# Kernel optimization log

Hardware: AMD Instinct MI355X
Metric: run time of the kernel (lower is better)

## Reference

```python
import jax, jax.numpy as jnp
import numpy as np
import math

B, L, D = 4, 4096, 512
P, V = 128, 8  # n_phases, value_dim
PI = math.pi

def _lin(x, w, b):
    return x @ w + b

def _gelu(x):
    return jax.nn.gelu(x, approximate=False)  # torch default exact GELU

def setup_inputs() -> dict:
    key = jax.random.key(0)
    ks = iter(jax.random.split(key, 32))
    def rn(shape, scale=0.02):
        return (jax.random.normal(next(ks), shape, dtype=jnp.float32) * scale)
    inp = {
        'x': jax.random.normal(next(ks), (B, L, D), dtype=jnp.float32),
        'pos_phases': jax.random.normal(next(ks), (L, D), dtype=jnp.float32) * PI,
        'magnitude_scale': jnp.float32(5.0),
        'w_v': rn((D, D)), 'b_v': jnp.zeros((D,), jnp.float32),
        'w_o': rn((D, D)), 'b_o': jnp.zeros((D,), jnp.float32),
        'w_m': rn((D, D)), 'b_m': jnp.zeros((D,), jnp.float32),
        'w_q': rn((D, D)), 'b_q': jnp.zeros((D,), jnp.float32),
        'w_ke': rn((D, P)), 'b_ke': jnp.zeros((P,), jnp.float32),
        'w_ve': rn((D, V)), 'b_ve': jnp.zeros((V,), jnp.float32),
        'w_s1': rn((2 * D, D)), 'b_s1': jnp.zeros((D,), jnp.float32),
        'w_s2': rn((D, P)), 'b_s2': jnp.zeros((P,), jnp.float32),
        'w_g': rn((D, 1)), 'b_g': jnp.zeros((1,), jnp.float32),
        'w_kv': rn((V, D)), 'b_kv': jnp.zeros((D,), jnp.float32),
        'ln_g': jnp.ones((2 * D,), jnp.float32), 'ln_b': jnp.zeros((2 * D,), jnp.float32),
        'w_t1': rn((2 * D, 2 * D)), 'b_t1': jnp.zeros((2 * D,), jnp.float32),
        'w_t2': rn((2 * D, D)), 'b_t2': jnp.zeros((D,), jnp.float32),
    }
    return inp

def _forward(x, pos_phases, magnitude_scale, w_v, b_v, w_o, b_o, w_m, b_m,
             w_q, b_q, w_ke, b_ke, w_ve, b_ve, w_s1, b_s1, w_s2, b_s2,
             w_g, b_g, w_kv, b_kv, ln_g, ln_b, w_t1, b_t1, w_t2, b_t2):
    b, l, d = x.shape
    phi = pos_phases[:l]                               # [L,D]
    cos_phi, sin_phi = jnp.cos(phi), jnp.sin(phi)
    # --- positional phasor memory ---
    v1 = _lin(x, w_v, b_v)                             # [B,L,D]
    magnitude = jax.nn.sigmoid(_lin(x, w_m, b_m)) * jnp.abs(magnitude_scale)
    weighted_v1 = magnitude * v1
    mem1_cos = jnp.cumsum(weighted_v1 * cos_phi, axis=1)
    mem1_sin = jnp.cumsum(weighted_v1 * sin_phi, axis=1)
    sqrt_mag = jnp.sqrt(jnp.cumsum(magnitude, axis=1) + 1e-8)
    mem1_cos = mem1_cos / sqrt_mag
    mem1_sin = mem1_sin / sqrt_mag
    phi_query = phi + _lin(x, w_q, b_q)
    pos_ret = (mem1_cos * jnp.cos(phi_query) + mem1_sin * jnp.sin(phi_query)) / math.sqrt(d)
    pos_out = _lin(pos_ret, w_o, b_o)                  # [B,L,D]
    # --- key-value phasor memory ---
    query_phase = jnp.tanh(_lin(x, w_ke, b_ke)) * PI   # [B,L,P]
    values = _lin(x, w_ve, b_ve)                       # [B,L,V]
    store_gate = jax.nn.sigmoid(_lin(x, w_g, b_g))     # [B,L,1]
    positions = jnp.arange(1, l + 1, dtype=x.dtype)[None, :, None]
    context_avg = jnp.cumsum(x, axis=1) / positions
    sk = _lin(_gelu(_lin(jnp.concatenate([x, context_avg], axis=-1), w_s1, b_s1)), w_s2, b_s2)
    storage_phase = jnp.tanh(sk) * PI                  # [B,L,P]
    gv = values * store_gate                           # [B,L,V]
    kv_bound_cos = jnp.cos(storage_phase)[..., None] * gv[:, :, None, :]  # [B,L,P,V]
    kv_bound_sin = jnp.sin(storage_phase)[..., None] * gv[:, :, None, :]
    kv_mem_cos = jnp.cumsum(kv_bound_cos, axis=1)
    kv_mem_sin = jnp.cumsum(kv_bound_sin, axis=1)
    gate_cumsum = jnp.clip(jnp.cumsum(store_gate, axis=1), 1.0, None)     # [B,L,1]
    inv = 1.0 / jnp.sqrt(gate_cumsum)[..., None]
    kv_mem_cos = kv_mem_cos * inv
    kv_mem_sin = kv_mem_sin * inv
    kv_retrieved = (jnp.cos(query_phase)[..., None] * kv_mem_cos
                    + jnp.sin(query_phase)[..., None] * kv_mem_sin).sum(axis=2) / math.sqrt(P)
    kv_out = _lin(kv_retrieved, w_kv, b_kv)            # [B,L,D]
    # --- output projection (dropout = eval/identity) ---
    combined = jnp.concatenate([pos_out, kv_out], axis=-1)  # [B,L,2D]
    mu = combined.mean(axis=-1, keepdims=True)
    var = combined.var(axis=-1, keepdims=True)
    ln = (combined - mu) / jnp.sqrt(var + 1e-5) * ln_g + ln_b
    return x + _lin(_gelu(_lin(ln, w_t1, b_t1)), w_t2, b_t2)

def reference(x, pos_phases, magnitude_scale, w_v, b_v, w_o, b_o, w_m, b_m,
              w_q, b_q, w_ke, b_ke, w_ve, b_ve, w_s1, b_s1, w_s2, b_s2,
              w_g, b_g, w_kv, b_kv, ln_g, ln_b, w_t1, b_t1, w_t2, b_t2):
    return _forward(x, pos_phases, magnitude_scale, w_v, b_v, w_o, b_o, w_m, b_m,
                    w_q, b_q, w_ke, b_ke, w_ve, b_ve, w_s1, b_s1, w_s2, b_s2,
                    w_g, b_g, w_kv, b_kv, ln_g, ln_b, w_t1, b_t1, w_t2, b_t2)
```

## Files before the change

### kernel.cpp

```cpp
#include <hip/hip_runtime.h>
#include <math.h>

#define NTOK 16384
#define LSEQ 4096
#define BATCH 4
#define DDIM 512
#define PDIM 128
#define VDIM 8
#define PI_F 3.14159265358979323846f

#define NC2 64
#define CL2 64
#define NC3 128
#define CL3 32

#define VMQ_S 1536

typedef __attribute__((ext_vector_type(8))) short bfrag8;
typedef __attribute__((ext_vector_type(4))) float facc4;

__device__ __forceinline__ float sigmoid_(float v) { return 1.0f / (1.0f + expf(-v)); }
__device__ __forceinline__ float gelu_(float v) { return 0.5f * v * (1.0f + erff(v * 0.70710678118654752f)); }

__device__ __forceinline__ unsigned short f2bf(float f) {
    unsigned int u = __builtin_bit_cast(unsigned int, f);
    u += 0x7fffu + ((u >> 16) & 1u);
    return (unsigned short)(u >> 16);
}
__device__ __forceinline__ float bf2f(unsigned short h) {
    return __builtin_bit_cast(float, ((unsigned int)h) << 16);
}
__device__ __forceinline__ float bflo(unsigned int w) { return __builtin_bit_cast(float, w << 16); }
__device__ __forceinline__ float bfhi(unsigned int w) { return __builtin_bit_cast(float, w & 0xffff0000u); }

__device__ __forceinline__ void async16(const unsigned short* g, unsigned short* l) {
    __builtin_amdgcn_global_load_lds(
        (const __attribute__((address_space(1))) unsigned int*)g,
        (__attribute__((address_space(3))) unsigned int*)l, 16, 0, 0);
}

__global__ __launch_bounds__(256) void gemm_bf16(
    const unsigned short* __restrict__ A, int ldA,
    const unsigned short* __restrict__ Wt,
    const float* __restrict__ bias, int K,
    float* __restrict__ Cf, unsigned short* __restrict__ Cb, int ldC, int colOff,
    const float* __restrict__ res, int ldRes,
    int act)
{
    __shared__ __align__(16) unsigned short Asm[2][128 * 64];
    __shared__ __align__(16) unsigned short Bsm[2][128 * 64];
    const int tid = threadIdx.x;
    const int lane = tid & 63;
    const int wv = tid >> 6;
    const int wm = wv & 1, wn = wv >> 1;
    const int quad = lane >> 4, cc = lane & 15;

    const int C = gridDim.x, R = gridDim.y;
    const int bid = blockIdx.x + C * blockIdx.y;
    const int xcd = bid & 7;
    const int s = bid >> 3;
    const int by = xcd * (R >> 3) + s / C;
    const int bx = s - (s / C) * C;
    const int row0 = by << 7;
    const int col0 = bx << 7;

    facc4 acc[4][4];
#pragma unroll
    for (int i = 0; i < 4; ++i)
#pragma unroll
        for (int j = 0; j < 4; ++j) acc[i][j] = (facc4){0.f, 0.f, 0.f, 0.f};

    const int nk = K >> 6;

    int srow[4]; int soff[4]; int sdst[4];
#pragma unroll
    for (int k = 0; k < 4; ++k) {
        int g = tid + k * 256;
        int r = g >> 3, sd = g & 7;
        srow[k] = r;
        soff[k] = (sd ^ (r & 7)) * 8;
        sdst[k] = g * 8;
    }

    auto stage = [&](int t, int buf) {
        const int koff = t << 6;
#pragma unroll
        for (int k = 0; k < 4; ++k) {
            async16(A  + (size_t)(row0 + srow[k]) * ldA + koff + soff[k], &Asm[buf][sdst[k]]);
            async16(Wt + (size_t)(col0 + srow[k]) * K   + koff + soff[k], &Bsm[buf][sdst[k]]);
        }
    };

    stage(0, 0);

    const int swz = cc & 7;
    int cur = 0;
    for (int t = 0; t < nk; ++t) {
        if (t + 1 < nk) {
            stage(t + 1, cur ^ 1);
            asm volatile("s_waitcnt vmcnt(8)" ::: "memory");
        } else {
            asm volatile("s_waitcnt vmcnt(0)" ::: "memory");
        }
        __builtin_amdgcn_s_barrier();
        __builtin_amdgcn_sched_barrier(0);
#pragma unroll
        for (int kk = 0; kk < 2; ++kk) {
            const int sl = ((kk * 4 + quad) ^ swz) * 8;
            bfrag8 afr[4], bfr[4];
#pragma unroll
            for (int mt = 0; mt < 4; ++mt)
                afr[mt] = *(const bfrag8*)&Asm[cur][(wm * 64 + mt * 16 + cc) * 64 + sl];
#pragma unroll
            for (int nt = 0; nt < 4; ++nt)
                bfr[nt] = *(const bfrag8*)&Bsm[cur][(wn * 64 + nt * 16 + cc) * 64 + sl];
#pragma unroll
            for (int mt = 0; mt < 4; ++mt)
#pragma unroll
                for (int nt = 0; nt < 4; ++nt)
                    acc[mt][nt] = __builtin_amdgcn_mfma_f32_16x16x32_bf16(
                        afr[mt], bfr[nt], acc[mt][nt], 0, 0, 0);
        }
        asm volatile("s_waitcnt lgkmcnt(0)" ::: "memory");
        __builtin_amdgcn_s_barrier();
        cur ^= 1;
    }

#pragma unroll
    for (int nt = 0; nt < 4; ++nt) {
        int col = col0 + wn * 64 + nt * 16 + cc;
        float bvv = bias[col];
#pragma unroll
        for (int mt = 0; mt < 4; ++mt) {
            int rowb = row0 + wm * 64 + mt * 16 + quad * 4;
#pragma unroll
            for (int r = 0; r < 4; ++r) {
                float v = acc[mt][nt][r] + bvv;
                if (act == 1) v = gelu_(v);
                size_t row = (size_t)(rowb + r);
                if (res) v += res[row * ldRes + col];
                size_t idx = row * ldC + colOff + col;
                if (Cf) Cf[idx] = v;
                else    Cb[idx] = f2bf(v);
            }
        }
    }
}

__global__ __launch_bounds__(256) void k_wcvt_all(
    const float* __restrict__ w_v, const float* __restrict__ w_m,
    const float* __restrict__ w_q, const float* __restrict__ w_o,
    const float* __restrict__ w_ke, const float* __restrict__ w_s1,
    const float* __restrict__ w_s2, const float* __restrict__ w_t1,
    const float* __restrict__ w_t2, unsigned short* __restrict__ WT,
    const float* __restrict__ b_v, const float* __restrict__ b_m,
    const float* __restrict__ b_q, float* __restrict__ cbias)
{
    const int bid = blockIdx.x;
    const int tid = threadIdx.x;
    if (bid >= 3200) {
        int i = (bid - 3200) * 256 + tid;
        if (i < 512) cbias[i] = b_v[i];
        else if (i < 1024) cbias[i] = b_m[i - 512];
        else cbias[i] = b_q[i - 1024];
        return;
    }
    const float* W; int K, N; unsigned short* Wt; int l;
    if (bid < 1024) {
        K = 512; N = 512;
        int seg = bid >> 8; l = bid & 255;
        W = (seg == 0) ? w_v : (seg == 1) ? w_m : (seg == 2) ? w_q : w_o;
        Wt = WT + seg * 262144;
    } else if (bid < 1088) { W = w_ke; K = 512;  N = 128;  Wt = WT + 1048576; l = bid - 1024; }
    else if (bid < 1600)   { W = w_s1; K = 1024; N = 512;  Wt = WT + 1114112; l = bid - 1088; }
    else if (bid < 1664)   { W = w_s2; K = 512;  N = 128;  Wt = WT + 1638400; l = bid - 1600; }
    else if (bid < 2688)   { W = w_t1; K = 1024; N = 1024; Wt = WT + 1703936; l = bid - 1664; }
    else                   { W = w_t2; K = 1024; N = 512;  Wt = WT + 2752512; l = bid - 2688; }
    const int ntx = N >> 5;
    const int bx = l % ntx, by = l / ntx;
    __shared__ float t[32][33];
    const int tx = tid & 31, ty = tid >> 5;
#pragma unroll
    for (int r = 0; r < 4; ++r) {
        int k = by * 32 + ty + r * 8;
        t[ty + r * 8][tx] = W[(size_t)k * N + bx * 32 + tx];
    }
    __syncthreads();
#pragma unroll
    for (int r = 0; r < 4; ++r) {
        int n = bx * 32 + ty + r * 8;
        Wt[(size_t)n * K + by * 32 + tx] = f2bf(t[tx][ty + r * 8]);
    }
}

__global__ void k_xcvt(const float* __restrict__ x, unsigned short* __restrict__ xcat)
{
    int g = blockIdx.x * 256 + threadIdx.x;
    int c8 = (g & 63) * 8, r = g >> 6;
    const float4* xp = (const float4*)(x + (size_t)r * 512 + c8);
    float4 a = xp[0], b = xp[1];
    uint4 o;
    o.x = (unsigned int)f2bf(a.x) | ((unsigned int)f2bf(a.y) << 16);
    o.y = (unsigned int)f2bf(a.z) | ((unsigned int)f2bf(a.w) << 16);
    o.z = (unsigned int)f2bf(b.x) | ((unsigned int)f2bf(b.y) << 16);
    o.w = (unsigned int)f2bf(b.z) | ((unsigned int)f2bf(b.w) << 16);
    *(uint4*)&xcat[(size_t)r * 1024 + c8] = o;
}

__global__ void k_phi(const float* __restrict__ pp, float* __restrict__ cphi,
                      float* __restrict__ sphi, int n)
{
    int i = blockIdx.x * 256 + threadIdx.x;
    if (i < n) {
        float s, c;
        sincosf(pp[i], &s, &c);
        cphi[i] = c;
        sphi[i] = s;
    }
}

__global__ __launch_bounds__(256) void k_glin(const float* __restrict__ x,
                                              const float* __restrict__ wg,
                                              const float* __restrict__ bg,
                                              float* __restrict__ glin)
{
    int wid = threadIdx.x >> 6, lane = threadIdx.x & 63;
    int row = blockIdx.x * 4 + wid;
    const float4* xr = (const float4*)(x + (size_t)row * DDIM);
    const float4* w4 = (const float4*)wg;
    float4 a0 = xr[lane], a1 = xr[lane + 64];
    float4 w0 = w4[lane], w1 = w4[lane + 64];
    float p = a0.x * w0.x + a0.y * w0.y + a0.z * w0.z + a0.w * w0.w
            + a1.x * w1.x + a1.y * w1.y + a1.z * w1.z + a1.w * w1.w;
    for (int d = 32; d >= 1; d >>= 1) p += __shfl_down(p, d, 64);
    if (lane == 0) glin[row] = p + bg[0];
}

__global__ __launch_bounds__(256) void k_values(const float* __restrict__ x,
                                                const float* __restrict__ wve,
                                                const float* __restrict__ bve,
                                                const float* __restrict__ glin,
                                                float* __restrict__ gv)
{
    int g = blockIdx.x * 256 + threadIdx.x;
    int m = g & 7, r = g >> 3;
    const float4* xr = (const float4*)(x + (size_t)r * DDIM);
    float acc = bve[m];
    for (int kq = 0; kq < 128; ++kq) {
        float4 a = xr[kq];
        int k = kq * 4;
        acc += a.x * wve[k * 8 + m] + a.y * wve[(k + 1) * 8 + m]
             + a.z * wve[(k + 2) * 8 + m] + a.w * wve[(k + 3) * 8 + m];
    }
    gv[g] = acc * sigmoid_(glin[r]);
}

__global__ __launch_bounds__(256) void k_scan1a(
    const unsigned short* __restrict__ vmq, const float* __restrict__ x,
    const float* __restrict__ cphi, const float* __restrict__ sphi,
    const float* __restrict__ msp, float* __restrict__ sum2)
{
    int g = blockIdx.x * 256 + threadIdx.x;
    int d = g & 511;
    int rest = g >> 9;
    int chunk = rest & (NC2 - 1);
    int b = rest >> 6;
    float msabs = fabsf(msp[0]);
    size_t row = (size_t)b * LSEQ + chunk * CL2;
    const unsigned short* vp = vmq + row * VMQ_S + d;
    const float* xp = x + row * DDIM + d;
    size_t pbase = ((size_t)chunk * CL2) * DDIM + d;
    float ac = 0.f, as = 0.f, am = 0.f, ax = 0.f;
    for (int i = 0; i < CL2; ++i) {
        float vv = bf2f(vp[0]);
        float ml = bf2f(vp[512]);
        float xv = xp[0];
        float cp = cphi[pbase], sp = sphi[pbase];
        float mag = msabs * sigmoid_(ml);
        float wv = mag * vv;
        ac += wv * cp; as += wv * sp; am += mag; ax += xv;
        vp += VMQ_S; xp += DDIM; pbase += DDIM;
    }
    int col = (b * DDIM + d) * NC2 + chunk;
    sum2[0 * 131072 + col] = ac;
    sum2[1 * 131072 + col] = as;
    sum2[2 * 131072 + col] = am;
    sum2[3 * 131072 + col] = ax;
}

__global__ __launch_bounds__(256) void k_scan1b(float* __restrict__ sum2)
{
    int g = blockIdx.x * 256 + threadIdx.x;
    float* p = sum2 + (size_t)g * NC2;
    float run = 0.f;
    for (int i = 0; i < NC2; ++i) { float t = p[i]; p[i] = run; run += t; }
}

__global__ __launch_bounds__(256) void k_scan1c(
    const unsigned short* __restrict__ vmq, const float* __restrict__ x,
    const float* __restrict__ cphi, const float* __restrict__ sphi,
    const float* __restrict__ msp, const float* __restrict__ sum2,
    unsigned short* __restrict__ pret, unsigned short* __restrict__ xcat)
{
    int g = blockIdx.x * 256 + threadIdx.x;
    int d = g & 511;
    int rest = g >> 9;
    int chunk = rest & (NC2 - 1);
    int b = rest >> 6;
    float msabs = fabsf(msp[0]);
    int col = (b * DDIM + d) * NC2 + chunk;
    float ac = sum2[col];
    float as = sum2[131072 + col];
    float am = sum2[2 * 131072 + col];
    float ax = sum2[3 * 131072 + col];
    size_t row = (size_t)b * LSEQ + chunk * CL2;
    const unsigned short* vp = vmq + row * VMQ_S + d;
    size_t base = row * DDIM + d;
    size_t pbase = ((size_t)chunk * CL2) * DDIM + d;
    int l = chunk * CL2;
    const float rsd = 0.04419417382415922f;
    for (int i = 0; i < CL2; ++i, ++l) {
        float vv = bf2f(vp[0]);
        float ml = bf2f(vp[512]);
        float q = bf2f(vp[1024]);
        float xv = x[base];
        float cp = cphi[pbase], sp = sphi[pbase];
        float mag = msabs * sigmoid_(ml);
        float wv = mag * vv;
        ac += wv * cp; as += wv * sp; am += mag; ax += xv;
        float inv = rsqrtf(am + 1e-8f);
        float mc = ac * inv, msn = as * inv;
        float cq, sq;
        sincosf(q, &sq, &cq);
        float cpq = cp * cq - sp * sq;
        float spq = sp * cq + cp * sq;
        pret[base] = f2bf((mc * cpq + msn * spq) * rsd);
        size_t orow = (size_t)b * LSEQ + l;
        xcat[orow * 1024 + 512 + d] = f2bf(ax / (float)(l + 1));
        vp += VMQ_S; base += DDIM; pbase += DDIM;
    }
}

__global__ void k_phases(const float* __restrict__ sk, const unsigned short* __restrict__ ke,
                         unsigned short* __restrict__ csp, unsigned short* __restrict__ ssp,
                         unsigned short* __restrict__ cqp, unsigned short* __restrict__ sqp, int n)
{
    int g = blockIdx.x * 256 + threadIdx.x;
    if (g < n) {
        float s, c;
        float spv = tanhf(sk[g]) * PI_F;
        sincosf(spv, &s, &c);
        csp[g] = f2bf(c); ssp[g] = f2bf(s);
        float qpv = tanhf(bf2f(ke[g])) * PI_F;
        sincosf(qpv, &s, &c);
        cqp[g] = f2bf(c); sqp[g] = f2bf(s);
    }
}

__global__ __launch_bounds__(1024) void k_gatescan(const float* __restrict__ glin,
                                                   float* __restrict__ gcum)
{
    __shared__ float s[1024];
    int b = blockIdx.x, tid = threadIdx.x;
    const float* gp = glin + (size_t)b * LSEQ + tid * 4;
    float e0 = sigmoid_(gp[0]);
    float e1 = sigmoid_(gp[1]);
    float e2 = sigmoid_(gp[2]);
    float e3 = sigmoid_(gp[3]);
    float l0 = e0, l1 = l0 + e1, l2 = l1 + e2, l3 = l2 + e3;
    s[tid] = l3;
    __syncthreads();
    for (int off = 1; off < 1024; off <<= 1) {
        float t = (tid >= off) ? s[tid - off] : 0.0f;
        __syncthreads();
        s[tid] += t;
        __syncthreads();
    }
    float excl = s[tid] - l3;
    float* out = gcum + (size_t)b * LSEQ + tid * 4;
    out[0] = excl + l0; out[1] = excl + l1; out[2] = excl + l2; out[3] = excl + l3;
}

__device__ __forceinline__ size_t kv_sum_idx(int b, int p, int v) {
    return ((((size_t)b * PDIM + p) * VDIM + v) * 2) * NC3;
}

__global__ __launch_bounds__(256) void k_kv1(const unsigned short* __restrict__ csp,
                                             const unsigned short* __restrict__ ssp,
                                             const float* __restrict__ gv,
                                             float* __restrict__ sum3)
{
    int blk = blockIdx.x;
    int chunk = blk & (NC3 - 1), b = blk >> 7;
    int tid = threadIdx.x;
    int w = tid >> 6, lane = tid & 63;
    int v = 2 * w + (lane & 1);
    int pq = lane >> 1;
    float sc[4] = {0, 0, 0, 0}, ss[4] = {0, 0, 0, 0};
    const uint2* c2p = (const uint2*)csp;
    const uint2* s2p = (const uint2*)ssp;
    int t = b * LSEQ + chunk * CL3;
    for (int i = 0; i < CL3; ++i, ++t) {
        uint2 cu = c2p[(size_t)t * 32 + pq];
        uint2 su = s2p[(size_t)t * 32 + pq];
        float g = gv[(size_t)t * VDIM + v];
        sc[0] += bflo(cu.x) * g; sc[1] += bfhi(cu.x) * g;
        sc[2] += bflo(cu.y) * g; sc[3] += bfhi(cu.y) * g;
        ss[0] += bflo(su.x) * g; ss[1] += bfhi(su.x) * g;
        ss[2] += bflo(su.y) * g; ss[3] += bfhi(su.y) * g;
    }
#pragma unroll
    for (int j = 0; j < 4; ++j) {
        size_t base = kv_sum_idx(b, pq * 4 + j, v) + chunk;
        sum3[base] = sc[j];
        sum3[base + NC3] = ss[j];
    }
}

__global__ __launch_bounds__(256) void k_kv2(float* __restrict__ sum3)
{
    int g = blockIdx.x * 256 + threadIdx.x;
    float* p = sum3 + (size_t)g * NC3;
    float run = 0.f;
    for (int i = 0; i < NC3; ++i) { float t = p[i]; p[i] = run; run += t; }
}

__global__ __launch_bounds__(256) void k_kv3(const unsigned short* __restrict__ csp,
                                             const unsigned short* __restrict__ ssp,
                                             const unsigned short* __restrict__ cqp,
                                             const unsigned short* __restrict__ sqp,
                                             const float* __restrict__ gv,
                                             const float* __restrict__ gcum,
                                             const float* __restrict__ sum3,
                                             float* __restrict__ kvr)
{
    int blk = blockIdx.x;
    int chunk = blk & (NC3 - 1), b = blk >> 7;
    int tid = threadIdx.x;
    int w = tid >> 6, lane = tid & 63;
    int v = 2 * w + (lane & 1);
    int pq = lane >> 1;
    float sc[4], ss[4];
#pragma unroll
    for (int j = 0; j < 4; ++j) {
        size_t base = kv_sum_idx(b, pq * 4 + j, v) + chunk;
        sc[j] = sum3[base];
        ss[j] = sum3[base + NC3];
    }
    const uint2* c2p = (const uint2*)csp;
    const uint2* s2p = (const uint2*)ssp;
    const uint2* cq2p = (const uint2*)cqp;
    const uint2* sq2p = (const uint2*)sqp;
    const float rsp = 0.08838834764831845f;
    int t = b * LSEQ + chunk * CL3;
    for (int i = 0; i < CL3; ++i, ++t) {
        uint2 cu = c2p[(size_t)t * 32 + pq];
        uint2 su = s2p[(size_t)t * 32 + pq];
        float g = gv[(size_t)t * VDIM + v];
        sc[0] += bflo(cu.x) * g; sc[1] += bfhi(cu.x) * g;
        sc[2] += bflo(cu.y) * g; sc[3] += bfhi(cu.y) * g;
        ss[0] += bflo(su.x) * g; ss[1] += bfhi(su.x) * g;
        ss[2] += bflo(su.y) * g; ss[3] += bfhi(su.y) * g;
        uint2 qcu = cq2p[(size_t)t * 32 + pq];
        uint2 qsu = sq2p[(size_t)t * 32 + pq];
        float part = bflo(qcu.x) * sc[0] + bfhi(qcu.x) * sc[1]
                   + bflo(qcu.y) * sc[2] + bfhi(qcu.y) * sc[3]
                   + bflo(qsu.x) * ss[0] + bfhi(qsu.x) * ss[1]
                   + bflo(qsu.y) * ss[2] + bfhi(qsu.y) * ss[3];
        part += __shfl_down(part, 32, 64);
        part += __shfl_down(part, 16, 64);
        part += __shfl_down(part, 8, 64);
        part += __shfl_down(part, 4, 64);
        part += __shfl_down(part, 2, 64);
        if (lane < 2) {
            float gc = gcum[t];
            float scale = rsqrtf(fmaxf(gc, 1.0f)) * rsp;
            kvr[(size_t)t * VDIM + v] = part * scale;
        }
    }
}

__global__ __launch_bounds__(256) void k_kvout(const float* __restrict__ kvr,
                                               const float* __restrict__ wkv,
                                               const float* __restrict__ bkv,
                                               unsigned short* __restrict__ comb)
{
    int g = blockIdx.x * 256 + threadIdx.x;
    int c8 = (g & 63) * 8, r = g >> 6;
    const float* kr = kvr + (size_t)r * VDIM;
    float k0 = kr[0], k1 = kr[1], k2 = kr[2], k3 = kr[3];
    float k4 = kr[4], k5 = kr[5], k6 = kr[6], k7 = kr[7];
    unsigned int o[4];
#pragma unroll
    for (int jj = 0; jj < 4; ++jj) {
        unsigned int w2 = 0;
#pragma unroll
        for (int h = 0; h < 2; ++h) {
            int c = c8 + jj * 2 + h;
            float acc = bkv[c];
            acc += k0 * wkv[0 * DDIM + c] + k1 * wkv[1 * DDIM + c]
                 + k2 * wkv[2 * DDIM + c] + k3 * wkv[3 * DDIM + c]
                 + k4 * wkv[4 * DDIM + c] + k5 * wkv[5 * DDIM + c]
                 + k6 * wkv[6 * DDIM + c] + k7 * wkv[7 * DDIM + c];
            w2 |= ((unsigned int)f2bf(acc)) << (16 * h);
        }
        o[jj] = w2;
    }
    *(uint4*)&comb[(size_t)r * 1024 + 512 + c8] = make_uint4(o[0], o[1], o[2], o[3]);
}

__global__ __launch_bounds__(256) void k_ln(unsigned short* __restrict__ comb,
                                            const float* __restrict__ gam,
                                            const float* __restrict__ bet)
{
    int wid = threadIdx.x >> 6, lane = threadIdx.x & 63;
    int row = blockIdx.x * 4 + wid;
    unsigned int* rp = (unsigned int*)(comb + (size_t)row * 1024);
    uint4 u0 = *(uint4*)&rp[lane * 8];
    uint4 u1 = *(uint4*)&rp[lane * 8 + 4];
    unsigned int uu[8] = {u0.x, u0.y, u0.z, u0.w, u1.x, u1.y, u1.z, u1.w};
    float v[16];
    float s = 0.f, s2 = 0.f;
#pragma unroll
    for (int j = 0; j < 8; ++j) {
        v[2 * j] = bflo(uu[j]);
        v[2 * j + 1] = bfhi(uu[j]);
        s += v[2 * j] + v[2 * j + 1];
        s2 += v[2 * j] * v[2 * j] + v[2 * j + 1] * v[2 * j + 1];
    }
    for (int m = 32; m >= 1; m >>= 1) {
        s += __shfl_xor(s, m, 64);
        s2 += __shfl_xor(s2, m, 64);
    }
    float mu = s * (1.0f / 1024.0f);
    float var = s2 * (1.0f / 1024.0f) - mu * mu;
    float inv = rsqrtf(var + 1e-5f);
    int c0 = lane * 16;
    unsigned int ou[8];
#pragma unroll
    for (int j = 0; j < 8; ++j) {
        float g0 = gam[c0 + 2 * j], g1 = gam[c0 + 2 * j + 1];
        float b0 = bet[c0 + 2 * j], b1 = bet[c0 + 2 * j + 1];
        float o0 = (v[2 * j] - mu) * inv * g0 + b0;
        float o1 = (v[2 * j + 1] - mu) * inv * g1 + b1;
        ou[j] = (unsigned int)f2bf(o0) | ((unsigned int)f2bf(o1) << 16);
    }
    *(uint4*)&rp[lane * 8] = make_uint4(ou[0], ou[1], ou[2], ou[3]);
    *(uint4*)&rp[lane * 8 + 4] = make_uint4(ou[4], ou[5], ou[6], ou[7]);
}

extern "C" void kernel_launch(void* const* d_in, const int* in_sizes, int n_in,
                              void* d_out, int out_size, void* d_ws, size_t ws_size,
                              hipStream_t stream)
{
    const float* x    = (const float*)d_in[0];
    const float* pp   = (const float*)d_in[1];
    const float* msp  = (const float*)d_in[2];
    const float* w_v  = (const float*)d_in[3];
    const float* b_v  = (const float*)d_in[4];
    const float* w_o  = (const float*)d_in[5];
    const float* b_o  = (const float*)d_in[6];
    const float* w_m  = (const float*)d_in[7];
    const float* b_m  = (const float*)d_in[8];
    const float* w_q  = (const float*)d_in[9];
    const float* b_q  = (const float*)d_in[10];
    const float* w_ke = (const float*)d_in[11];
    const float* b_ke = (const float*)d_in[12];
    const float* w_ve = (const float*)d_in[13];
    const float* b_ve = (const float*)d_in[14];
    const float* w_s1 = (const float*)d_in[15];
    const float* b_s1 = (const float*)d_in[16];
    const float* w_s2 = (const float*)d_in[17];
    const float* b_s2 = (const float*)d_in[18];
    const float* w_g  = (const float*)d_in[19];
    const float* b_g  = (const float*)d_in[20];
    const float* w_kv = (const float*)d_in[21];
    const float* b_kv = (const float*)d_in[22];
    const float* ln_g = (const float*)d_in[23];
    const float* ln_b = (const float*)d_in[24];
    const float* w_t1 = (const float*)d_in[25];
    const float* b_t1 = (const float*)d_in[26];
    const float* w_t2 = (const float*)d_in[27];
    const float* b_t2 = (const float*)d_in[28];
    float* out = (float*)d_out;
    float* ws = (float*)d_ws;
    (void)ws_size; (void)n_in; (void)in_sizes; (void)out_size;

    unsigned short* VMQ    = (unsigned short*)(ws);
    float*          SKf    = ws + 4194304;
    unsigned short* CSP    = (unsigned short*)(ws + 8388608);
    unsigned short* SSP    = CSP + 2097152;
    unsigned short* CQP    = CSP + 2 * 2097152;
    unsigned short* SQP    = CSP + 3 * 2097152;
    unsigned short* KEbf   = (unsigned short*)(ws + 12582912);
    float* GVb   = ws + 13631488;
    float* GLINb = ws + 13762560;
    float* GCUMb = ws + 13778944;
    float* SUM2b = ws + 13795328;
    float* CBIAS = SUM2b;
    float* SUM3b = ws + 14319616;
    float* KVRb  = ws + 15368192;
    float* CPHIb = ws + 15499264;
    float* SPHIb = ws + 17596416;
    unsigned short* HSbf   = (unsigned short*)(ws + 15499264);
    unsigned short* PRETbf = (unsigned short*)(ws + 19693568);
    unsigned short* XCAT   = (unsigned short*)(ws + 23887872);
    unsigned short* COMBbf = XCAT;
    unsigned short* HTbf   = (unsigned short*)(ws);
    unsigned short* WT     = (unsigned short*)(ws + 32276480);
    unsigned short* wv_t  = WT;
    unsigned short* wke_t = WT + 1048576;
    unsigned short* ws1_t = WT + 1114112;
    unsigned short* ws2_t = WT + 1638400;
    unsigned short* wt1_t = WT + 1703936;
    unsigned short* wt2_t = WT + 2752512;
    unsigned short* wo_t  = WT + 786432;

    k_phi<<<8192, 256, 0, stream>>>(pp, CPHIb, SPHIb, 2097152);
    k_xcvt<<<4096, 256, 0, stream>>>(x, XCAT);
    k_wcvt_all<<<3206, 256, 0, stream>>>(w_v, w_m, w_q, w_o, w_ke, w_s1, w_s2,
                                         w_t1, w_t2, WT, b_v, b_m, b_q, CBIAS);

    gemm_bf16<<<dim3(12, 128), 256, 0, stream>>>(XCAT, 1024, wv_t, CBIAS, 512, nullptr, VMQ, VMQ_S, 0, nullptr, 0, 0);
    gemm_bf16<<<dim3(1, 128), 256, 0, stream>>>(XCAT, 1024, wke_t, b_ke, 512, nullptr, KEbf, 128, 0, nullptr, 0, 0);
    k_glin<<<4096, 256, 0, stream>>>(x, w_g, b_g, GLINb);
    k_values<<<512, 256, 0, stream>>>(x, w_ve, b_ve, GLINb, GVb);

    k_scan1a<<<512, 256, 0, stream>>>(VMQ, x, CPHIb, SPHIb, msp, SUM2b);
    k_scan1b<<<32, 256, 0, stream>>>(SUM2b);
    k_scan1c<<<512, 256, 0, stream>>>(VMQ, x, CPHIb, SPHIb, msp, SUM2b, PRETbf, XCAT);

    gemm_bf16<<<dim3(4, 128), 256, 0, stream>>>(XCAT, 1024, ws1_t, b_s1, 1024, nullptr, HSbf, 512, 0, nullptr, 0, 1);
    gemm_bf16<<<dim3(1, 128), 256, 0, stream>>>(HSbf, 512, ws2_t, b_s2, 512, SKf, nullptr, 128, 0, nullptr, 0, 0);

    k_phases<<<8192, 256, 0, stream>>>(SKf, KEbf, CSP, SSP, CQP, SQP, 2097152);
    k_gatescan<<<4, 1024, 0, stream>>>(GLINb, GCUMb);

    k_kv1<<<512, 256, 0, stream>>>(CSP, SSP, GVb, SUM3b);
    k_kv2<<<32, 256, 0, stream>>>(SUM3b);
    k_kv3<<<512, 256, 0, stream>>>(CSP, SSP, CQP, SQP, GVb, GCUMb, SUM3b, KVRb);

    gemm_bf16<<<dim3(4, 128), 256, 0, stream>>>(PRETbf, 512, wo_t, b_o, 512, nullptr, COMBbf, 1024, 0, nullptr, 0, 0);
    k_kvout<<<4096, 256, 0, stream>>>(KVRb, w_kv, b_kv, COMBbf);
    k_ln<<<4096, 256, 0, stream>>>(COMBbf, ln_g, ln_b);
    gemm_bf16<<<dim3(8, 128), 256, 0, stream>>>(COMBbf, 1024, wt1_t, b_t1, 1024, nullptr, HTbf, 1024, 0, nullptr, 0, 1);
    gemm_bf16<<<dim3(4, 128), 256, 0, stream>>>(HTbf, 1024, wt2_t, b_t2, 1024, out, nullptr, 512, 0, x, 512, 0);
}
```

Baseline: 565.9 us.

## Fuse small kernels: merge ke into VMQ GEMM, inline sincos, fuse kvout+LN, glin+values

Folds the w_ke projection into the wide V/M/Q GEMM as a thirteenth column tile that writes to a second output buffer. The separate cos/sin precompute kernel is removed and sincosf is computed inline in the scan kernels, and the phase-plus-query rotation becomes a single sincosf of the summed angle. The gate-linear and value projection kernels become one per-row wave kernel, and the kv output projection is merged into LayerNorm. The aim is fewer launches and fewer global round trips, at the cost of redundant sincos work in two scan passes and a slightly different rounding path.

Result: slower. 590.6 us (+4.4%).

```diff
diff --git a/kernel.cpp b/kernel.cpp
--- a/kernel.cpp
+++ b/kernel.cpp
@@ -44,6 +44,7 @@
     const unsigned short* __restrict__ Wt,
     const float* __restrict__ bias, int K,
     float* __restrict__ Cf, unsigned short* __restrict__ Cb, int ldC, int colOff,
+    unsigned short* __restrict__ Cb2, int ldC2, int n1,
     const float* __restrict__ res, int ldRes,
     int act)
 {
@@ -126,6 +127,7 @@
         cur ^= 1;
     }
 
+    const bool sec = (Cb2 != nullptr) && (col0 >= n1);
 #pragma unroll
     for (int nt = 0; nt < 4; ++nt) {
         int col = col0 + wn * 64 + nt * 16 + cc;
@@ -139,9 +141,9 @@
                 if (act == 1) v = gelu_(v);
                 size_t row = (size_t)(rowb + r);
                 if (res) v += res[row * ldRes + col];
-                size_t idx = row * ldC + colOff + col;
-                if (Cf) Cf[idx] = v;
-                else    Cb[idx] = f2bf(v);
+                if (Cf) Cf[row * ldC + colOff + col] = v;
+                else if (sec) Cb2[row * ldC2 + (col - n1)] = f2bf(v);
+                else Cb[row * ldC + colOff + col] = f2bf(v);
             }
         }
     }
@@ -154,7 +156,8 @@
     const float* __restrict__ w_s2, const float* __restrict__ w_t1,
     const float* __restrict__ w_t2, unsigned short* __restrict__ WT,
     const float* __restrict__ b_v, const float* __restrict__ b_m,
-    const float* __restrict__ b_q, float* __restrict__ cbias)
+    const float* __restrict__ b_q, const float* __restrict__ b_ke,
+    float* __restrict__ cbias)
 {
     const int bid = blockIdx.x;
     const int tid = threadIdx.x;
@@ -162,16 +165,18 @@
         int i = (bid - 3200) * 256 + tid;
         if (i < 512) cbias[i] = b_v[i];
         else if (i < 1024) cbias[i] = b_m[i - 512];
-        else cbias[i] = b_q[i - 1024];
+        else if (i < 1536) cbias[i] = b_q[i - 1024];
+        else if (i < 1664) cbias[i] = b_ke[i - 1536];
         return;
     }
     const float* W; int K, N; unsigned short* Wt; int l;
-    if (bid < 1024) {
+    if (bid < 768) {
         K = 512; N = 512;
         int seg = bid >> 8; l = bid & 255;
-        W = (seg == 0) ? w_v : (seg == 1) ? w_m : (seg == 2) ? w_q : w_o;
+        W = (seg == 0) ? w_v : (seg == 1) ? w_m : w_q;
         Wt = WT + seg * 262144;
-    } else if (bid < 1088) { W = w_ke; K = 512;  N = 128;  Wt = WT + 1048576; l = bid - 1024; }
+    } else if (bid < 832)  { W = w_ke; K = 512;  N = 128;  Wt = WT + 786432;  l = bid - 768; }
+    else if (bid < 1088)   { W = w_o;  K = 512;  N = 512;  Wt = WT + 851968;  l = bid - 832; }
     else if (bid < 1600)   { W = w_s1; K = 1024; N = 512;  Wt = WT + 1114112; l = bid - 1088; }
     else if (bid < 1664)   { W = w_s2; K = 512;  N = 128;  Wt = WT + 1638400; l = bid - 1600; }
     else if (bid < 2688)   { W = w_t1; K = 1024; N = 1024; Wt = WT + 1703936; l = bid - 1664; }
@@ -207,22 +212,11 @@
     *(uint4*)&xcat[(size_t)r * 1024 + c8] = o;
 }
 
-__global__ void k_phi(const float* __restrict__ pp, float* __restrict__ cphi,
-                      float* __restrict__ sphi, int n)
-{
-    int i = blockIdx.x * 256 + threadIdx.x;
-    if (i < n) {
-        float s, c;
-        sincosf(pp[i], &s, &c);
-        cphi[i] = c;
-        sphi[i] = s;
-    }
-}
-
-__global__ __launch_bounds__(256) void k_glin(const float* __restrict__ x,
-                                              const float* __restrict__ wg,
-                                              const float* __restrict__ bg,
-                                              float* __restrict__ glin)
+__global__ __launch_bounds__(256) void k_glinval(
+    const float* __restrict__ x, const float* __restrict__ wg,
+    const float* __restrict__ bg, const float* __restrict__ wve,
+    const float* __restrict__ bve, float* __restrict__ glin,
+    float* __restrict__ gv)
 {
     int wid = threadIdx.x >> 6, lane = threadIdx.x & 63;
     int row = blockIdx.x * 4 + wid;
@@ -232,32 +226,38 @@
     float4 w0 = w4[lane], w1 = w4[lane + 64];
     float p = a0.x * w0.x + a0.y * w0.y + a0.z * w0.z + a0.w * w0.w
             + a1.x * w1.x + a1.y * w1.y + a1.z * w1.z + a1.w * w1.w;
-    for (int d = 32; d >= 1; d >>= 1) p += __shfl_down(p, d, 64);
-    if (lane == 0) glin[row] = p + bg[0];
-}
-
-__global__ __launch_bounds__(256) void k_values(const float* __restrict__ x,
-                                                const float* __restrict__ wve,
-                                                const float* __restrict__ bve,
-                                                const float* __restrict__ glin,
-                                                float* __restrict__ gv)
-{
-    int g = blockIdx.x * 256 + threadIdx.x;
-    int m = g & 7, r = g >> 3;
-    const float4* xr = (const float4*)(x + (size_t)r * DDIM);
-    float acc = bve[m];
-    for (int kq = 0; kq < 128; ++kq) {
-        float4 a = xr[kq];
-        int k = kq * 4;
-        acc += a.x * wve[k * 8 + m] + a.y * wve[(k + 1) * 8 + m]
-             + a.z * wve[(k + 2) * 8 + m] + a.w * wve[(k + 3) * 8 + m];
-    }
-    gv[g] = acc * sigmoid_(glin[r]);
+    float vm[8];
+#pragma unroll
+    for (int m = 0; m < 8; ++m) vm[m] = 0.f;
+    const float4* wv4 = (const float4*)wve;
+    float xa[8] = {a0.x, a0.y, a0.z, a0.w, a1.x, a1.y, a1.z, a1.w};
+#pragma unroll
+    for (int j = 0; j < 8; ++j) {
+        int krow = (j < 4) ? (4 * lane + j) : (256 + 4 * lane + (j - 4));
+        float4 wlo = wv4[krow * 2], whi = wv4[krow * 2 + 1];
+        float xv = xa[j];
+        vm[0] += xv * wlo.x; vm[1] += xv * wlo.y; vm[2] += xv * wlo.z; vm[3] += xv * wlo.w;
+        vm[4] += xv * whi.x; vm[5] += xv * whi.y; vm[6] += xv * whi.z; vm[7] += xv * whi.w;
+    }
+#pragma unroll
+    for (int d = 32; d >= 1; d >>= 1) {
+        p += __shfl_xor(p, d, 64);
+#pragma unroll
+        for (int m = 0; m < 8; ++m) vm[m] += __shfl_xor(vm[m], d, 64);
+    }
+    if (lane == 0) {
+        float gl = p + bg[0];
+        glin[row] = gl;
+        float sg = sigmoid_(gl);
+        float* gp = gv + (size_t)row * VDIM;
+#pragma unroll
+        for (int m = 0; m < 8; ++m) gp[m] = (vm[m] + bve[m]) * sg;
+    }
 }
 
 __global__ __launch_bounds__(256) void k_scan1a(
     const unsigned short* __restrict__ vmq, const float* __restrict__ x,
-    const float* __restrict__ cphi, const float* __restrict__ sphi,
+    const float* __restrict__ pp,
     const float* __restrict__ msp, float* __restrict__ sum2)
 {
     int g = blockIdx.x * 256 + threadIdx.x;
@@ -275,7 +275,8 @@
         float vv = bf2f(vp[0]);
         float ml = bf2f(vp[512]);
         float xv = xp[0];
-        float cp = cphi[pbase], sp = sphi[pbase];
+        float sp, cp;
+        sincosf(pp[pbase], &sp, &cp);
         float mag = msabs * sigmoid_(ml);
         float wv = mag * vv;
         ac += wv * cp; as += wv * sp; am += mag; ax += xv;
@@ -298,7 +299,7 @@
 
 __global__ __launch_bounds__(256) void k_scan1c(
     const unsigned short* __restrict__ vmq, const float* __restrict__ x,
-    const float* __restrict__ cphi, const float* __restrict__ sphi,
+    const float* __restrict__ pp,
     const float* __restrict__ msp, const float* __restrict__ sum2,
     unsigned short* __restrict__ pret, unsigned short* __restrict__ xcat)
 {
@@ -324,16 +325,16 @@
         float ml = bf2f(vp[512]);
         float q = bf2f(vp[1024]);
         float xv = x[base];
-        float cp = cphi[pbase], sp = sphi[pbase];
+        float ph = pp[pbase];
+        float sp, cp;
+        sincosf(ph, &sp, &cp);
         float mag = msabs * sigmoid_(ml);
         float wv = mag * vv;
         ac += wv * cp; as += wv * sp; am += mag; ax += xv;
         float inv = rsqrtf(am + 1e-8f);
         float mc = ac * inv, msn = as * inv;
-        float cq, sq;
-        sincosf(q, &sq, &cq);
-        float cpq = cp * cq - sp * sq;
-        float spq = sp * cq + cp * sq;
+        float spq, cpq;
+        sincosf(ph + q, &spq, &cpq);
         pret[base] = f2bf((mc * cpq + msn * spq) * rsd);
         size_t orow = (size_t)b * LSEQ + l;
         xcat[orow * 1024 + 512 + d] = f2bf(ax / (float)(l + 1));
@@ -480,53 +481,39 @@
     }
 }
 
-__global__ __launch_bounds__(256) void k_kvout(const float* __restrict__ kvr,
-                                               const float* __restrict__ wkv,
-                                               const float* __restrict__ bkv,
-                                               unsigned short* __restrict__ comb)
-{
-    int g = blockIdx.x * 256 + threadIdx.x;
-    int c8 = (g & 63) * 8, r = g >> 6;
-    const float* kr = kvr + (size_t)r * VDIM;
-    float k0 = kr[0], k1 = kr[1], k2 = kr[2], k3 = kr[3];
-    float k4 = kr[4], k5 = kr[5], k6 = kr[6], k7 = kr[7];
-    unsigned int o[4];
-#pragma unroll
-    for (int jj = 0; jj < 4; ++jj) {
-        unsigned int w2 = 0;
-#pragma unroll
-        for (int h = 0; h < 2; ++h) {
-            int c = c8 + jj * 2 + h;
-            float acc = bkv[c];
-            acc += k0 * wkv[0 * DDIM + c] + k1 * wkv[1 * DDIM + c]
-                 + k2 * wkv[2 * DDIM + c] + k3 * wkv[3 * DDIM + c]
-                 + k4 * wkv[4 * DDIM + c] + k5 * wkv[5 * DDIM + c]
-                 + k6 * wkv[6 * DDIM + c] + k7 * wkv[7 * DDIM + c];
-            w2 |= ((unsigned int)f2bf(acc)) << (16 * h);
-        }
-        o[jj] = w2;
-    }
-    *(uint4*)&comb[(size_t)r * 1024 + 512 + c8] = make_uint4(o[0], o[1], o[2], o[3]);
-}
-
-__global__ __launch_bounds__(256) void k_ln(unsigned short* __restrict__ comb,
-                                            const float* __restrict__ gam,
-                                            const float* __restrict__ bet)
+__global__ __launch_bounds__(256) void k_kvln(unsigned short* __restrict__ comb,
+                                              const float* __restrict__ kvr,
+                                              const float* __restrict__ wkv,
+                                              const float* __restrict__ bkv,
+                                              const float* __restrict__ gam,
+                                              const float* __restrict__ bet)
 {
     int wid = threadIdx.x >> 6, lane = threadIdx.x & 63;
     int row = blockIdx.x * 4 + wid;
     unsigned int* rp = (unsigned int*)(comb + (size_t)row * 1024);
-    uint4 u0 = *(uint4*)&rp[lane * 8];
-    uint4 u1 = *(uint4*)&rp[lane * 8 + 4];
-    unsigned int uu[8] = {u0.x, u0.y, u0.z, u0.w, u1.x, u1.y, u1.z, u1.w};
-    float v[16];
+    uint4 uL = *(uint4*)&rp[lane * 4];
+    float vl[8];
+    vl[0] = bflo(uL.x); vl[1] = bfhi(uL.x); vl[2] = bflo(uL.y); vl[3] = bfhi(uL.y);
+    vl[4] = bflo(uL.z); vl[5] = bfhi(uL.z); vl[6] = bflo(uL.w); vl[7] = bfhi(uL.w);
+    const float* kr = kvr + (size_t)row * VDIM;
+    float k0 = kr[0], k1 = kr[1], k2 = kr[2], k3 = kr[3];
+    float k4 = kr[4], k5 = kr[5], k6 = kr[6], k7 = kr[7];
+    int c0 = lane * 8;
+    float vr[8];
+#pragma unroll
+    for (int j = 0; j < 8; ++j) {
+        int c = c0 + j;
+        vr[j] = bkv[c]
+              + k0 * wkv[0 * DDIM + c] + k1 * wkv[1 * DDIM + c]
+              + k2 * wkv[2 * DDIM + c] + k3 * wkv[3 * DDIM + c]
+              + k4 * wkv[4 * DDIM + c] + k5 * wkv[5 * DDIM + c]
+              + k6 * wkv[6 * DDIM + c] + k7 * wkv[7 * DDIM + c];
+    }
     float s = 0.f, s2 = 0.f;
 #pragma unroll
     for (int j = 0; j < 8; ++j) {
-        v[2 * j] = bflo(uu[j]);
-        v[2 * j + 1] = bfhi(uu[j]);
-        s += v[2 * j] + v[2 * j + 1];
-        s2 += v[2 * j] * v[2 * j] + v[2 * j + 1] * v[2 * j + 1];
+        s += vl[j] + vr[j];
+        s2 += vl[j] * vl[j] + vr[j] * vr[j];
     }
     for (int m = 32; m >= 1; m >>= 1) {
         s += __shfl_xor(s, m, 64);
@@ -535,18 +522,19 @@
     float mu = s * (1.0f / 1024.0f);
     float var = s2 * (1.0f / 1024.0f) - mu * mu;
     float inv = rsqrtf(var + 1e-5f);
-    int c0 = lane * 16;
-    unsigned int ou[8];
-#pragma unroll
-    for (int j = 0; j < 8; ++j) {
-        float g0 = gam[c0 + 2 * j], g1 = gam[c0 + 2 * j + 1];
-        float b0 = bet[c0 + 2 * j], b1 = bet[c0 + 2 * j + 1];
-        float o0 = (v[2 * j] - mu) * inv * g0 + b0;
-        float o1 = (v[2 * j + 1] - mu) * inv * g1 + b1;
-        ou[j] = (unsigned int)f2bf(o0) | ((unsigned int)f2bf(o1) << 16);
-    }
-    *(uint4*)&rp[lane * 8] = make_uint4(ou[0], ou[1], ou[2], ou[3]);
-    *(uint4*)&rp[lane * 8 + 4] = make_uint4(ou[4], ou[5], ou[6], ou[7]);
+    unsigned int oL[4], oR[4];
+#pragma unroll
+    for (int jj = 0; jj < 4; ++jj) {
+        float l0 = (vl[2 * jj] - mu) * inv * gam[c0 + 2 * jj] + bet[c0 + 2 * jj];
+        float l1 = (vl[2 * jj + 1] - mu) * inv * gam[c0 + 2 * jj + 1] + bet[c0 + 2 * jj + 1];
+        oL[jj] = (unsigned int)f2bf(l0) | ((unsigned int)f2bf(l1) << 16);
+        int rc = 512 + c0 + 2 * jj;
+        float r0 = (vr[2 * jj] - mu) * inv * gam[rc] + bet[rc];
+        float r1 = (vr[2 * jj + 1] - mu) * inv * gam[rc + 1] + bet[rc + 1];
+        oR[jj] = (unsigned int)f2bf(r0) | ((unsigned int)f2bf(r1) << 16);
+    }
+    *(uint4*)&rp[lane * 4] = make_uint4(oL[0], oL[1], oL[2], oL[3]);
+    *(uint4*)&rp[256 + lane * 4] = make_uint4(oR[0], oR[1], oR[2], oR[3]);
 }
 
 extern "C" void kernel_launch(void* const* d_in, const int* in_sizes, int n_in,
@@ -600,8 +588,6 @@
     float* CBIAS = SUM2b;
     float* SUM3b = ws + 14319616;
     float* KVRb  = ws + 15368192;
-    float* CPHIb = ws + 15499264;
-    float* SPHIb = ws + 17596416;
     unsigned short* HSbf   = (unsigned short*)(ws + 15499264);
     unsigned short* PRETbf = (unsigned short*)(ws + 19693568);
     unsigned short* XCAT   = (unsigned short*)(ws + 23887872);
@@ -609,29 +595,28 @@
     unsigned short* HTbf   = (unsigned short*)(ws);
     unsigned short* WT     = (unsigned short*)(ws + 32276480);
     unsigned short* wv_t  = WT;
-    unsigned short* wke_t = WT + 1048576;
+    unsigned short* wo_t  = WT + 851968;
     unsigned short* ws1_t = WT + 1114112;
     unsigned short* ws2_t = WT + 1638400;
     unsigned short* wt1_t = WT + 1703936;
     unsigned short* wt2_t = WT + 2752512;
-    unsigned short* wo_t  = WT + 786432;
-
-    k_phi<<<8192, 256, 0, stream>>>(pp, CPHIb, SPHIb, 2097152);
+
     k_xcvt<<<4096, 256, 0, stream>>>(x, XCAT);
-    k_wcvt_all<<<3206, 256, 0, stream>>>(w_v, w_m, w_q, w_o, w_ke, w_s1, w_s2,
-                                         w_t1, w_t2, WT, b_v, b_m, b_q, CBIAS);
-
-    gemm_bf16<<<dim3(12, 128), 256, 0, stream>>>(XCAT, 1024, wv_t, CBIAS, 512, nullptr, VMQ, VMQ_S, 0, nullptr, 0, 0);
-    gemm_bf16<<<dim3(1, 128), 256, 0, stream>>>(XCAT, 1024, wke_t, b_ke, 512, nullptr, KEbf, 128, 0, nullptr, 0, 0);
-    k_glin<<<4096, 256, 0, stream>>>(x, w_g, b_g, GLINb);
-    k_values<<<512, 256, 0, stream>>>(x, w_ve, b_ve, GLINb, GVb);
-
-    k_scan1a<<<512, 256, 0, stream>>>(VMQ, x, CPHIb, SPHIb, msp, SUM2b);
+    k_wcvt_all<<<3207, 256, 0, stream>>>(w_v, w_m, w_q, w_o, w_ke, w_s1, w_s2,
+                                         w_t1, w_t2, WT, b_v, b_m, b_q, b_ke, CBIAS);
+
+    gemm_bf16<<<dim3(13, 128), 256, 0, stream>>>(XCAT, 1024, wv_t, CBIAS, 512,
+        nullptr, VMQ, VMQ_S, 0, KEbf, PDIM, 1536, nullptr, 0, 0);
+    k_glinval<<<4096, 256, 0, stream>>>(x, w_g, b_g, w_ve, b_ve, GLINb, GVb);
+
+    k_scan1a<<<512, 256, 0, stream>>>(VMQ, x, pp, msp, SUM2b);
     k_scan1b<<<32, 256, 0, stream>>>(SUM2b);
-    k_scan1c<<<512, 256, 0, stream>>>(VMQ, x, CPHIb, SPHIb, msp, SUM2b, PRETbf, XCAT);
-
-    gemm_bf16<<<dim3(4, 128), 256, 0, stream>>>(XCAT, 1024, ws1_t, b_s1, 1024, nullptr, HSbf, 512, 0, nullptr, 0, 1);
-    gemm_bf16<<<dim3(1, 128), 256, 0, stream>>>(HSbf, 512, ws2_t, b_s2, 512, SKf, nullptr, 128, 0, nullptr, 0, 0);
+    k_scan1c<<<512, 256, 0, stream>>>(VMQ, x, pp, msp, SUM2b, PRETbf, XCAT);
+
+    gemm_bf16<<<dim3(4, 128), 256, 0, stream>>>(XCAT, 1024, ws1_t, b_s1, 1024,
+        nullptr, HSbf, 512, 0, nullptr, 0, 0, nullptr, 0, 1);
+    gemm_bf16<<<dim3(1, 128), 256, 0, stream>>>(HSbf, 512, ws2_t, b_s2, 512,
+        SKf, nullptr, 128, 0, nullptr, 0, 0, nullptr, 0, 0);
 
     k_phases<<<8192, 256, 0, stream>>>(SKf, KEbf, CSP, SSP, CQP, SQP, 2097152);
     k_gatescan<<<4, 1024, 0, stream>>>(GLINb, GCUMb);
@@ -640,9 +625,11 @@
     k_kv2<<<32, 256, 0, stream>>>(SUM3b);
     k_kv3<<<512, 256, 0, stream>>>(CSP, SSP, CQP, SQP, GVb, GCUMb, SUM3b, KVRb);
 
-    gemm_bf16<<<dim3(4, 128), 256, 0, stream>>>(PRETbf, 512, wo_t, b_o, 512, nullptr, COMBbf, 1024, 0, nullptr, 0, 0);
-    k_kvout<<<4096, 256, 0, stream>>>(KVRb, w_kv, b_kv, COMBbf);
-    k_ln<<<4096, 256, 0, stream>>>(COMBbf, ln_g, ln_b);
-    gemm_bf16<<<dim3(8, 128), 256, 0, stream>>>(COMBbf, 1024, wt1_t, b_t1, 1024, nullptr, HTbf, 1024, 0, nullptr, 0, 1);
-    gemm_bf16<<<dim3(4, 128), 256, 0, stream>>>(HTbf, 1024, wt2_t, b_t2, 1024, out, nullptr, 512, 0, x, 512, 0);
-}
+    gemm_bf16<<<dim3(4, 128), 256, 0, stream>>>(PRETbf, 512, wo_t, b_o, 512,
+        nullptr, COMBbf, 1024, 0, nullptr, 0, 0, nullptr, 0, 0);
+    k_kvln<<<4096, 256, 0, stream>>>(COMBbf, KVRb, w_kv, b_kv, ln_g, ln_b);
+    gemm_bf16<<<dim3(8, 128), 256, 0, stream>>>(COMBbf, 1024, wt1_t, b_t1, 1024,
+        nullptr, HTbf, 1024, 0, nullptr, 0, 0, nullptr, 0, 1);
+    gemm_bf16<<<dim3(4, 128), 256, 0, stream>>>(HTbf, 1024, wt2_t, b_t2, 1024,
+        out, nullptr, 512, 0, nullptr, 0, 0, x, 512, 0);
+}
```
